# Performance work log

Measured on AMD Instinct MI355X. Metric: run time of the kernel, lower is better.

The kernel has to match this reference:

```python
import jax, jax.numpy as jnp
import numpy as np

K = 5  # box-blur width along disparity axis

def _blur_disparity(x):
    # depthwise conv1d with ones(K)/K kernel, zero 'same' padding, along axis 1
    N, D, H, W = x.shape
    xp = jnp.pad(x, ((0, 0), (K // 2, K // 2), (0, 0), (0, 0)))
    acc = xp[:, 0:D]
    for s in range(1, K):
        acc = acc + xp[:, s:s + D]
    return acc / K

def _modal_mask(x):
    N, D, H, W = x.shape
    index = jnp.argmax(x, axis=1, keepdims=True)                 # [N,1,H,W] int
    d = jnp.arange(D, dtype=x.dtype).reshape(1, D, 1, 1)
    d2 = jnp.arange(D + 1, dtype=x.dtype).reshape(1, D + 1, 1, 1)
    ones = jnp.ones((N, 1, H, W), dtype=x.dtype)
    x_diff_r = jnp.diff(x, axis=1, prepend=ones, append=ones)    # [N,D+1,H,W]
    x_diff_l = jnp.diff(x, axis=1, prepend=ones)                 # [N,D,H,W]
    # right edge of dominant mode: first positive diff strictly right of peak
    ind_r = ((x_diff_r * (d2 > index)) > 0).astype(jnp.int32)
    index_r = jnp.argmax(ind_r, axis=1, keepdims=True) - 1
    # left edge: last negative diff at/left of peak
    ind_l = ((x_diff_l * (d <= index)) < 0).astype(jnp.int32)
    index_l = D - 1 - jnp.argmax(jnp.flip(ind_l, axis=1), axis=1, keepdims=True)
    mask1 = (d >= index_l) & (d <= index_r)
    r = jnp.minimum(index_r - index, index - index_l)
    mask2 = (d >= index - r) & (d <= index + r)
    valid = jnp.abs(2 * index - index_r - index_l) < 3           # near-symmetric mode
    return jnp.where(valid, mask1, mask2)                        # bool [N,D,H,W]

def setup_inputs() -> dict:
    key = jax.random.key(0)
    N, D, H, W = 2, 192, 256, 512
    x = jax.random.uniform(key, (N, D, H, W), dtype=jnp.float32)
    return {"x": x}

def reference(x) -> jnp.ndarray:
    N, D, H, W = x.shape
    disp = jnp.arange(D, dtype=x.dtype).reshape(1, D, 1, 1)
    x_blur = _blur_disparity(x)
    mask = _modal_mask(x_blur)
    y = x * mask                       # primary mode mass
    z = x - y
    x_blur2 = x_blur * (~mask)
    z = z * _modal_mask(x_blur2)       # secondary mode mass
    valid = (jnp.sum(y, axis=1) >= jnp.sum(z, axis=1)).astype(jnp.float32)[:, None]
    xm = valid * y + (1.0 - valid) * z
    xm = xm / jnp.sum(xm, axis=1, keepdims=True)
    out = jnp.sum(xm * disp, axis=1, keepdims=True)  # [N,1,H,W]
    return out
```

## Files before the change

kernel.cpp:

```cpp
#include <hip/hip_runtime.h>
#include <math.h>

namespace {
constexpr int D     = 192;
constexpr int HW    = 256 * 512;
constexpr int TOTAL = 2 * HW;

__device__ __forceinline__ float div5(float s) {
    const float c = 0.2f;
    float q = s * c;
    float r = __builtin_fmaf(-5.0f, q, s);
    return __builtin_fmaf(r, c, q);
}

__device__ __forceinline__ bool in_range(int d, int lo, unsigned width) {
    return (unsigned)(d - lo) <= width;
}

struct Machine {
    float bprev, maxv;
    int   index, last_fall, index_l, index_r;
    bool  r_found;

    __device__ __forceinline__ void init() {
        bprev = 1.0f;
        maxv  = -INFINITY;
        index = 0; last_fall = 0; index_l = 0;
        index_r = D - 1;
        r_found = false;
    }

    __device__ __forceinline__ void step(int d, float b) {
        float diff = b - bprev;
        bool fall  = diff < 0.0f;
        last_fall  = fall ? d : last_fall;
        bool am    = b > maxv;
        maxv       = am ? b : maxv;
        index      = am ? d : index;
        index_l    = am ? last_fall : index_l;
        bool rise  = (diff > 0.0f) & (!r_found) & (!am);
        index_r    = am ? (D - 1) : (rise ? (d - 1) : index_r);
        r_found    = am ? false : (r_found | rise);
        bprev      = b;
    }

    __device__ __forceinline__ void finish(int& lo, unsigned& wd) const {
        int r = min(index_r - index, index - index_l);
        int t = 2 * index - index_r - index_l;
        bool valid = (t > -3) && (t < 3);
        lo = valid ? index_l : (index - r);
        int hi = valid ? index_r : (index + r);
        wd = (unsigned)(hi - lo);
    }
};

template<int OFS>
__device__ __forceinline__ void loadc(const float* __restrict__ col, int c,
                                      float (&buf)[8]) {
    #pragma unroll
    for (int j = 0; j < 8; ++j)
        buf[j] = col[(size_t)(8 * c + OFS + j) * HW];
}
template<int OFS>
__device__ __forceinline__ void loadc_guard(const float* __restrict__ col, int c,
                                            float (&buf)[8]) {
    #pragma unroll
    for (int j = 0; j < 8; ++j) {
        int idx = 8 * c + OFS + j;
        buf[j] = (idx < D) ? col[(size_t)idx * HW] : 0.0f;
    }
}

template<int OFS, typename F>
__device__ __forceinline__ void stream24(const float* __restrict__ col, F&& f) {
    float A[8], B[8], C[8];
    loadc<OFS>(col, 0, A);
    loadc<OFS>(col, 1, B);
    loadc<OFS>(col, 2, C);
    int d = 0;
    auto comp = [&](float (&buf)[8]) {
        #pragma unroll
        for (int j = 0; j < 8; ++j) { f(d, buf[j]); ++d; }
    };
    for (int g = 0; g < 6; ++g) {
        comp(A); loadc<OFS>(col, 3 * g + 3, A);
        comp(B); loadc<OFS>(col, 3 * g + 4, B);
        comp(C); loadc<OFS>(col, 3 * g + 5, C);
    }
    comp(A); loadc<OFS>(col, 21, A);
    comp(B); loadc<OFS>(col, 22, B);
    comp(C);
    if (OFS == 2) loadc_guard<OFS>(col, 23, C);
    else          loadc<OFS>(col, 23, C);
    comp(A); comp(B); comp(C);
}
}

extern "C" __global__ void __launch_bounds__(256, 4)
dme_kernel(const float* __restrict__ x, float* __restrict__ out)
{
    const int n  = blockIdx.x >> 9;
    const int hw = ((blockIdx.x & 511) << 8) | threadIdx.x;
    const float* __restrict__ col = x + (size_t)n * (size_t)(D * HW) + hw;

    const float x0 = col[0];
    const float x1 = col[HW];

    Machine m1; m1.init();
    {
        float w0 = 0.f, w1 = 0.f, w2 = x0, w3 = x1;
        stream24<2>(col, [&](int d, float xv) {
            float s = w0 + w1; s += w2; s += w3; s += xv;
            m1.step(d, div5(s));
            w0 = w1; w1 = w2; w2 = w3; w3 = xv;
        });
    }
    int lo1; unsigned wd1; m1.finish(lo1, wd1);

    Machine m2; m2.init();
    float sum_y = 0.f, wsum_y = 0.f;
    {
        float w0 = 0.f, w1 = 0.f, w2 = x0, w3 = x1;
        float fd = 0.0f;
        stream24<2>(col, [&](int d, float xv) {
            float s = w0 + w1; s += w2; s += w3; s += xv;
            float b = div5(s);
            bool in1 = in_range(d, lo1, wd1);
            m2.step(d, in1 ? 0.0f : b);
            sum_y += in1 ? w2 : 0.f;
            float t = in1 ? fd : 0.f;
            wsum_y = __builtin_fmaf(t, w2, wsum_y);
            w0 = w1; w1 = w2; w2 = w3; w3 = xv; fd += 1.0f;
        });
    }
    int lo2; unsigned wd2; m2.finish(lo2, wd2);

    float sum_z = 0.f, wsum_z = 0.f;
    {
        const int dend = lo2 + (int)wd2;
        for (int d = lo2; d <= dend; ++d) {
            float xv = col[(size_t)d * HW];
            bool  zz = !in_range(d, lo1, wd1);
            float xm = zz ? xv : 0.0f;
            sum_z += xm;
            wsum_z = __builtin_fmaf(xm, (float)d, wsum_z);
        }
    }

    bool  v = (sum_y >= sum_z);
    float S = v ? sum_y  : sum_z;
    float W = v ? wsum_y : wsum_z;
    out[hw + n * HW] = W / S;
}

extern "C" void kernel_launch(void* const* d_in, const int* in_sizes, int n_in,
                              void* d_out, int out_size, void* d_ws, size_t ws_size,
                              hipStream_t stream)
{
    const float* x   = (const float*)d_in[0];
    float*       out = (float*)d_out;
    dim3 block(256), grid(TOTAL / 256);
    hipLaunchKernelGGL(dme_kernel, grid, block, 0, stream, x, out);
}
```

Baseline: 320.6 us.

## Stream columns through per-wave LDS ring via global_load_lds with async prefetch

Replaces register-buffered strided global loads with asynchronous global_load_lds into a 32-slot per-wave LDS ring, read back with inline-asm ds_read and manual vmcnt waits, to keep more loads in flight. It also moves the primary-mode sum and weighted sum out of the second streaming pass into a separate gather loop over the mask range, which shortens the second pass at the cost of extra global reads. The hand-written waitcnt and offset scheduling are fragile, and the extra LDS use may reduce occupancy.

```diff
diff --git a/kernel.cpp b/kernel.cpp
--- a/kernel.cpp
+++ b/kernel.cpp
@@ -5,6 +5,10 @@
 constexpr int D     = 192;
 constexpr int HW    = 256 * 512;
 constexpr int TOTAL = 2 * HW;
+constexpr unsigned ROWB = (unsigned)HW * 4u;
+constexpr int RING_B = 8192;
+
+typedef __attribute__((address_space(3))) char lds_char;
 
 __device__ __forceinline__ float div5(float s) {
     const float c = 0.2f;
@@ -54,62 +58,105 @@
     }
 };
 
-template<int OFS>
-__device__ __forceinline__ void loadc(const float* __restrict__ col, int c,
-                                      float (&buf)[8]) {
-    #pragma unroll
-    for (int j = 0; j < 8; ++j)
-        buf[j] = col[(size_t)(8 * c + OFS + j) * HW];
-}
-template<int OFS>
-__device__ __forceinline__ void loadc_guard(const float* __restrict__ col, int c,
-                                            float (&buf)[8]) {
+template<int C>
+__device__ __forceinline__ void issue8(const char* colb, lds_char* ldsb) {
     #pragma unroll
     for (int j = 0; j < 8; ++j) {
-        int idx = 8 * c + OFS + j;
-        buf[j] = (idx < D) ? col[(size_t)idx * HW] : 0.0f;
-    }
-}
-
-template<int OFS, typename F>
-__device__ __forceinline__ void stream24(const float* __restrict__ col, F&& f) {
-    float A[8], B[8], C[8];
-    loadc<OFS>(col, 0, A);
-    loadc<OFS>(col, 1, B);
-    loadc<OFS>(col, 2, C);
+        const int      el = 8 * C + j;
+        const int      gi = el + 2;
+        const unsigned bo = (gi < D) ? (unsigned)gi * ROWB : 0u;
+        __builtin_amdgcn_global_load_lds(
+            (__attribute__((address_space(1))) void*)(colb + bo),
+            (__attribute__((address_space(3))) void*)(ldsb + ((el & 31) << 8)),
+            4, 0, 0);
+    }
+}
+
+#define DS_RW(VM, O0,O1,O2,O3,O4,O5,O6,O7, B, VA)                         \
+    asm volatile("s_waitcnt vmcnt(" #VM ")\n\t"                           \
+                 "ds_read_b32 %0, %8 offset:" #O0 "\n\t"                  \
+                 "ds_read_b32 %1, %8 offset:" #O1 "\n\t"                  \
+                 "ds_read_b32 %2, %8 offset:" #O2 "\n\t"                  \
+                 "ds_read_b32 %3, %8 offset:" #O3 "\n\t"                  \
+                 "ds_read_b32 %4, %8 offset:" #O4 "\n\t"                  \
+                 "ds_read_b32 %5, %8 offset:" #O5 "\n\t"                  \
+                 "ds_read_b32 %6, %8 offset:" #O6 "\n\t"                  \
+                 "ds_read_b32 %7, %8 offset:" #O7 "\n\t"                  \
+                 "s_waitcnt lgkmcnt(0)"                                   \
+                 : "=&v"(B[0]), "=&v"(B[1]), "=&v"(B[2]), "=&v"(B[3]),    \
+                   "=&v"(B[4]), "=&v"(B[5]), "=&v"(B[6]), "=&v"(B[7])     \
+                 : "v"(VA) : "memory")
+
+#define RD0(VM,B,VA) DS_RW(VM,    0, 256, 512, 768,1024,1280,1536,1792,B,VA)
+#define RD1(VM,B,VA) DS_RW(VM, 2048,2304,2560,2816,3072,3328,3584,3840,B,VA)
+#define RD2(VM,B,VA) DS_RW(VM, 4096,4352,4608,4864,5120,5376,5632,5888,B,VA)
+#define RD3(VM,B,VA) DS_RW(VM, 6144,6400,6656,6912,7168,7424,7936-256,7936,B,VA)
+
+template<typename F>
+__device__ __forceinline__ void stream_ring(const char* colb, lds_char* ldsb,
+                                            unsigned va, F&& f) {
+    float B[8];
     int d = 0;
-    auto comp = [&](float (&buf)[8]) {
+    auto comp = [&]() {
         #pragma unroll
-        for (int j = 0; j < 8; ++j) { f(d, buf[j]); ++d; }
+        for (int j = 0; j < 8; ++j) {
+            float xv = B[j];
+            if (d >= 190) xv = 0.0f;
+            f(d, xv);
+            ++d;
+        }
     };
-    for (int g = 0; g < 6; ++g) {
-        comp(A); loadc<OFS>(col, 3 * g + 3, A);
-        comp(B); loadc<OFS>(col, 3 * g + 4, B);
-        comp(C); loadc<OFS>(col, 3 * g + 5, C);
-    }
-    comp(A); loadc<OFS>(col, 21, A);
-    comp(B); loadc<OFS>(col, 22, B);
-    comp(C);
-    if (OFS == 2) loadc_guard<OFS>(col, 23, C);
-    else          loadc<OFS>(col, 23, C);
-    comp(A); comp(B); comp(C);
+    issue8<0>(colb, ldsb); issue8<1>(colb, ldsb);
+    issue8<2>(colb, ldsb); issue8<3>(colb, ldsb);
+    RD0(24,B,va); comp(); issue8< 4>(colb, ldsb);
+    RD1(24,B,va); comp(); issue8< 5>(colb, ldsb);
+    RD2(24,B,va); comp(); issue8< 6>(colb, ldsb);
+    RD3(24,B,va); comp(); issue8< 7>(colb, ldsb);
+    RD0(24,B,va); comp(); issue8< 8>(colb, ldsb);
+    RD1(24,B,va); comp(); issue8< 9>(colb, ldsb);
+    RD2(24,B,va); comp(); issue8<10>(colb, ldsb);
+    RD3(24,B,va); comp(); issue8<11>(colb, ldsb);
+    RD0(24,B,va); comp(); issue8<12>(colb, ldsb);
+    RD1(24,B,va); comp(); issue8<13>(colb, ldsb);
+    RD2(24,B,va); comp(); issue8<14>(colb, ldsb);
+    RD3(24,B,va); comp(); issue8<15>(colb, ldsb);
+    RD0(24,B,va); comp(); issue8<16>(colb, ldsb);
+    RD1(24,B,va); comp(); issue8<17>(colb, ldsb);
+    RD2(24,B,va); comp(); issue8<18>(colb, ldsb);
+    RD3(24,B,va); comp(); issue8<19>(colb, ldsb);
+    RD0(24,B,va); comp(); issue8<20>(colb, ldsb);
+    RD1(24,B,va); comp(); issue8<21>(colb, ldsb);
+    RD2(24,B,va); comp(); issue8<22>(colb, ldsb);
+    RD3(24,B,va); comp(); issue8<23>(colb, ldsb);
+    RD0(24,B,va); comp();
+    RD1(16,B,va); comp();
+    RD2( 8,B,va); comp();
+    RD3( 0,B,va); comp();
 }
 }
 
 extern "C" __global__ void __launch_bounds__(256, 4)
 dme_kernel(const float* __restrict__ x, float* __restrict__ out)
 {
+    __shared__ char ring[4 * RING_B];
+
     const int n  = blockIdx.x >> 9;
     const int hw = ((blockIdx.x & 511) << 8) | threadIdx.x;
-    const float* __restrict__ col = x + (size_t)n * (size_t)(D * HW) + hw;
-
-    const float x0 = col[0];
-    const float x1 = col[HW];
+    const float* __restrict__ xn = x + (size_t)n * (size_t)(D * HW);
+    const char* colb = (const char*)xn + (unsigned)hw * 4u;
+
+    const int wid  = threadIdx.x >> 6;
+    const int lane = threadIdx.x & 63;
+    lds_char* ldsb = (lds_char*)&ring[wid * RING_B];
+    const unsigned va = (unsigned)(size_t)ldsb + (unsigned)lane * 4u;
+
+    const float x0 = *(const float*)colb;
+    const float x1 = *(const float*)(colb + ROWB);
 
     Machine m1; m1.init();
     {
         float w0 = 0.f, w1 = 0.f, w2 = x0, w3 = x1;
-        stream24<2>(col, [&](int d, float xv) {
+        stream_ring(colb, ldsb, va, [&](int d, float xv) {
             float s = w0 + w1; s += w2; s += w3; s += xv;
             m1.step(d, div5(s));
             w0 = w1; w1 = w2; w2 = w3; w3 = xv;
@@ -118,32 +165,37 @@
     int lo1; unsigned wd1; m1.finish(lo1, wd1);
 
     Machine m2; m2.init();
-    float sum_y = 0.f, wsum_y = 0.f;
     {
         float w0 = 0.f, w1 = 0.f, w2 = x0, w3 = x1;
-        float fd = 0.0f;
-        stream24<2>(col, [&](int d, float xv) {
+        stream_ring(colb, ldsb, va, [&](int d, float xv) {
             float s = w0 + w1; s += w2; s += w3; s += xv;
             float b = div5(s);
             bool in1 = in_range(d, lo1, wd1);
             m2.step(d, in1 ? 0.0f : b);
-            sum_y += in1 ? w2 : 0.f;
-            float t = in1 ? fd : 0.f;
-            wsum_y = __builtin_fmaf(t, w2, wsum_y);
-            w0 = w1; w1 = w2; w2 = w3; w3 = xv; fd += 1.0f;
+            w0 = w1; w1 = w2; w2 = w3; w3 = xv;
         });
     }
     int lo2; unsigned wd2; m2.finish(lo2, wd2);
 
+    float sum_y = 0.f, wsum_y = 0.f;
+    {
+        const int dend = lo1 + (int)wd1;
+        for (int dd = lo1; dd <= dend; ++dd) {
+            float xv = *(const float*)(colb + (unsigned)dd * ROWB);
+            sum_y += xv;
+            wsum_y = __builtin_fmaf(xv, (float)dd, wsum_y);
+        }
+    }
+
     float sum_z = 0.f, wsum_z = 0.f;
     {
         const int dend = lo2 + (int)wd2;
-        for (int d = lo2; d <= dend; ++d) {
-            float xv = col[(size_t)d * HW];
-            bool  zz = !in_range(d, lo1, wd1);
+        for (int dd = lo2; dd <= dend; ++dd) {
+            float xv = *(const float*)(colb + (unsigned)dd * ROWB);
+            bool  zz = !in_range(dd, lo1, wd1);
             float xm = zz ? xv : 0.0f;
             sum_z += xm;
-            wsum_z = __builtin_fmaf(xm, (float)d, wsum_z);
+            wsum_z = __builtin_fmaf(xm, (float)dd, wsum_z);
         }
     }
 
```

Result: slower. 881.8 us (+175.1%).
